# Kernel tuning notes

Hardware: AMD Instinct MI355X
Metric: run time of the kernel (lower is better)

The kernel has to match this reference:

```python
import jax, jax.numpy as jnp
import numpy as np

B, T, C, H = 1, 2048, 1024, 16
K = C // H


def _ln(x, g, b):
    m = x.mean(-1, keepdims=True)
    v = ((x - m) ** 2).mean(-1, keepdims=True)
    return (x - m) * jax.lax.rsqrt(v + 1e-5) * g + b


def setup_inputs() -> dict:
    key = jax.random.key(0)
    ks = jax.random.split(key, 16)
    n = lambda k, s, sc=1.0: jax.random.normal(k, s, jnp.float32) * sc
    u = lambda k, s: jax.random.uniform(k, s, jnp.float32)
    ws = C ** -0.5
    return {
        "x": n(ks[0], (B, T, C)),
        "shift_state": n(ks[1], (B, C)),
        "time_maa_x": u(ks[2], (1, 1, C)),
        "time_maa_r": u(ks[3], (1, 1, C)),
        "time_maa_k": u(ks[4], (1, 1, C)),
        "time_maa_v": u(ks[5], (1, 1, C)),
        "time_maa_w1": n(ks[6], (C, 96), 0.01),
        "time_maa_w2": n(ks[7], (3, 32, C), 0.01),
        "headavg_w1": n(ks[8], (C, 4 * 2 * H), 0.01),
        "headavg_w2": n(ks[9], (4, 2 * H, H), 0.01),
        "w_r": n(ks[10], (C, C), ws),
        "w_k": n(ks[11], (C, C), ws),
        "w_v": n(ks[12], (C, C), ws),
        "w_o": n(ks[13], (C, C), ws),
        "ln_r_g": jnp.ones((C,)), "ln_r_b": jnp.zeros((C,)),
        "ln_k_g": jnp.ones((C,)), "ln_k_b": jnp.zeros((C,)),
        "ln_v_g": jnp.ones((C,)), "ln_v_b": jnp.zeros((C,)),
        "ln_x_g": jnp.ones((C,)), "ln_x_b": jnp.zeros((C,)),
    }


def reference(x, shift_state, time_maa_x, time_maa_r, time_maa_k, time_maa_v,
              time_maa_w1, time_maa_w2, headavg_w1, headavg_w2,
              w_r, w_k, w_v, w_o,
              ln_r_g, ln_r_b, ln_k_g, ln_k_b, ln_v_g, ln_v_b, ln_x_g, ln_x_b):
    Bs, Ts, Cs = x.shape
    Hh = headavg_w2.shape[-1]
    Kk = Cs // Hh

    # token shift
    dxprev = jnp.concatenate([shift_state[:, None, :], x[:, :-1]], axis=1) - x

    # LoRA token-shift mixing
    xxx = jnp.tanh((x + dxprev * time_maa_x) @ time_maa_w1)       # [B,T,3*32]
    mix = jnp.einsum('btnd,ndc->nbtc', xxx.reshape(Bs, Ts, 3, -1), time_maa_w2)
    mq, mk, mv = mix[0], mix[1], mix[2]
    xq = x + dxprev * (time_maa_r + mq)
    xk = x + dxprev * (time_maa_k + mk)
    xv = x + dxprev * (time_maa_v + mv)

    q = _ln(xq @ w_r, ln_r_g, ln_r_b).reshape(Bs, Ts, Hh, Kk).transpose(0, 2, 1, 3)
    k = _ln(xk @ w_k, ln_k_g, ln_k_b).reshape(Bs, Ts, Hh, Kk).transpose(0, 2, 1, 3)
    v = _ln(xv @ w_v, ln_v_g, ln_v_b).reshape(Bs, Ts, Hh, Kk).transpose(0, 2, 1, 3)

    # per-head LoRA score mixing coefficients
    ha = jnp.tanh(x @ headavg_w1).reshape(Bs, Ts, 4, -1)          # [B,T,4,2H]
    hm = jnp.einsum('btnd,ndh->nbth', ha, headavg_w2) / Hh        # [4,B,T,H]
    pre_q, pre_k, post_q, post_k = hm[0], hm[1], hm[2], hm[3]

    scale = Kk ** -0.5
    y = jnp.einsum('bhtk,bhsk->bhts', q * scale, k)               # [B,H,T,S]
    y = y + jnp.einsum('bhts,bth->bts', y, pre_q)[:, None]
    y = y + jnp.einsum('bhts,bsh->bts', y, pre_k)[:, None]

    # causal ALiBi bias
    rel = (jnp.arange(Ts)[:, None] - jnp.arange(Ts)[None, :]).astype(x.dtype)
    slopes = (2.0 ** (-8.0 * jnp.arange(1, Hh + 1, dtype=x.dtype) / Hh))
    bias = jnp.where(rel >= 0, -slopes[:, None, None] * rel, jnp.asarray(-1e9, x.dtype))
    y = y + bias[None]

    y = jax.nn.softmax(y, axis=-1)
    y = y + jnp.einsum('bhts,bth->bts', y, post_q)[:, None]
    y = y + jnp.einsum('bhts,bsh->bts', y, post_k)[:, None]

    out = jnp.einsum('bhts,bhsv->bhtv', y, v).transpose(0, 2, 1, 3).reshape(Bs, Ts, Cs)
    out = _ln(out, ln_x_g, ln_x_b) @ w_o
    return out
```

## Files before the change

kernel.cpp:

```cpp
#include <hip/hip_runtime.h>
#include <cstdint>
#include <cstddef>


#define C_DIM 1024
#define HEADS 16
#define TTL 32
#define STL 32
#define SCHUNK 256
#define PADS 40
#define EPS_STR 36

typedef unsigned short ushort_t;
typedef __attribute__((ext_vector_type(8))) short bf16x8;
typedef __attribute__((ext_vector_type(4))) float f32x4;

#define MFMA16(a, b, c) __builtin_amdgcn_mfma_f32_16x16x32_bf16(a, b, c, 0, 0, 0)

__device__ __forceinline__ unsigned int f2bf_u(float f) {
  unsigned int u = __float_as_uint(f);
  return (u + 0x7fffu + ((u >> 16) & 1u)) >> 16;
}
__device__ __forceinline__ float bf2f(ushort_t u) {
  return __uint_as_float(((unsigned int)u) << 16);
}
__device__ __forceinline__ void pack4(ushort_t* dst, float x0, float x1,
                                      float x2, float x3) {
  uint2 v;
  v.x = f2bf_u(x0) | (f2bf_u(x1) << 16);
  v.y = f2bf_u(x2) | (f2bf_u(x3) << 16);
  *(uint2*)dst = v;
}
__device__ __forceinline__ void mlmerge(float& M, float& L, float m2, float l2) {
  float nm = fmaxf(M, m2);
  float ea = (M  <= -1e29f) ? 0.f : __expf(M - nm);
  float eb = (m2 <= -1e29f) ? 0.f : __expf(m2 - nm);
  L = L * ea + l2 * eb;
  M = nm;
}

__global__ __launch_bounds__(256) void prep_kernel(
    const float* __restrict__ x, const float* __restrict__ shift,
    const float* __restrict__ maa_x,
    float* __restrict__ dxprev, ushort_t* __restrict__ zbf,
    ushort_t* __restrict__ xbf)
{
  const int t = blockIdx.x;
  const int c = threadIdx.x * 4;
  const size_t base = (size_t)t * C_DIM + c;
  const float4 xc = *(const float4*)&x[base];
  const float4 xp = (t == 0) ? *(const float4*)&shift[c]
                             : *(const float4*)&x[base - C_DIM];
  const float4 mx = *(const float4*)&maa_x[c];
  float4 d;
  d.x = xp.x - xc.x; d.y = xp.y - xc.y; d.z = xp.z - xc.z; d.w = xp.w - xc.w;
  *(float4*)&dxprev[base] = d;
  pack4(&zbf[base], xc.x + d.x*mx.x, xc.y + d.y*mx.y,
        xc.z + d.z*mx.z, xc.w + d.w*mx.w);
  pack4(&xbf[base], xc.x, xc.y, xc.z, xc.w);
}

__global__ __launch_bounds__(256) void wlora_prep(
    const float* __restrict__ w1, const float* __restrict__ hw1,
    ushort_t* __restrict__ wlt)
{
  __shared__ float tile[32][33];
  const int k0 = blockIdx.x*32, j0 = blockIdx.y*32;
  const int r = threadIdx.x >> 3, c4 = (threadIdx.x & 7) * 4;
  const float* W = (j0 < 96) ? w1 : hw1;
  const int stride = (j0 < 96) ? 96 : 128;
  const int jo = (j0 < 96) ? j0 : j0 - 96;
  const float4 v = *(const float4*)&W[(size_t)(k0+r)*stride + jo + c4];
  tile[r][c4+0] = v.x; tile[r][c4+1] = v.y;
  tile[r][c4+2] = v.z; tile[r][c4+3] = v.w;
  __syncthreads();
  pack4(&wlt[(size_t)(j0+r)*C_DIM + k0 + c4],
        tile[c4+0][r], tile[c4+1][r], tile[c4+2][r], tile[c4+3][r]);
}

__global__ __launch_bounds__(64) void lora_gemm(
    const ushort_t* __restrict__ zbf, const ushort_t* __restrict__ xbf,
    const ushort_t* __restrict__ wlt, float* __restrict__ xxx,
    float* __restrict__ ha)
{
  const int nt = blockIdx.y;
  const int bm = blockIdx.x * 32;
  const ushort_t* A = (nt < 3) ? zbf : xbf;
  const int wrow = nt * 32;
  const int lane = threadIdx.x;
  const int l15 = lane & 15, g = lane >> 4;
  f32x4 acc[2][2];
  #pragma unroll
  for (int i = 0; i < 2; i++)
    #pragma unroll
    for (int j = 0; j < 2; j++) acc[i][j] = (f32x4){0.f,0.f,0.f,0.f};
  bf16x8 a0[2], b0[2], a1[2], b1[2];
  #define LLA(dst, kk) { \
    dst[0] = *(const bf16x8*)&A[(size_t)(bm + l15)*C_DIM + (kk) + g*8]; \
    dst[1] = *(const bf16x8*)&A[(size_t)(bm + 16 + l15)*C_DIM + (kk) + g*8]; }
  #define LLB(dst, kk) { \
    dst[0] = *(const bf16x8*)&wlt[(size_t)(wrow + l15)*C_DIM + (kk) + g*8]; \
    dst[1] = *(const bf16x8*)&wlt[(size_t)(wrow + 16 + l15)*C_DIM + (kk) + g*8]; }
  LLA(a0, 0); LLB(b0, 0);
  for (int k0 = 0; k0 < C_DIM; k0 += 64) {
    LLA(a1, k0+32); LLB(b1, k0+32);
    #pragma unroll
    for (int i = 0; i < 2; i++)
      #pragma unroll
      for (int j = 0; j < 2; j++) acc[i][j] = MFMA16(a0[i], b0[j], acc[i][j]);
    if (k0 + 64 < C_DIM) { LLA(a0, k0+64); LLB(b0, k0+64); }
    #pragma unroll
    for (int i = 0; i < 2; i++)
      #pragma unroll
      for (int j = 0; j < 2; j++) acc[i][j] = MFMA16(a1[i], b1[j], acc[i][j]);
  }
  #undef LLA
  #undef LLB
  #pragma unroll
  for (int i = 0; i < 2; i++)
    #pragma unroll
    for (int j = 0; j < 2; j++)
      #pragma unroll
      for (int r = 0; r < 4; r++) {
        const int t = bm + i*16 + g*4 + r;
        const int col = wrow + j*16 + l15;
        const float val = tanhf(acc[i][j][r]);
        if (nt < 3) xxx[(size_t)t*96 + col] = val;
        else        ha[(size_t)t*128 + col - 96] = val;
      }
}

__global__ __launch_bounds__(256) void mix_kernel(
    const float* __restrict__ x, const float* __restrict__ dxp,
    const float* __restrict__ xxx,
    const float* __restrict__ maa_r, const float* __restrict__ maa_k,
    const float* __restrict__ maa_v, const float* __restrict__ w2,
    ushort_t* __restrict__ xq, ushort_t* __restrict__ xk,
    ushort_t* __restrict__ xv)
{
  __shared__ float xs[8][96];
  const int t0 = blockIdx.x * 8;
  const int tid = threadIdx.x;
  #pragma unroll
  for (int i = 0; i < 3; i++) {
    const int u = tid + i*256;
    if (u < 768) {
      const int r = u / 96, cc = u % 96;
      xs[r][cc] = xxx[(size_t)(t0+r)*96 + cc];
    }
  }
  __syncthreads();
  const int c = tid * 4;
  float4 xc[8], dx[8];
  #pragma unroll
  for (int r = 0; r < 8; r++) {
    xc[r] = *(const float4*)&x[(size_t)(t0+r)*C_DIM + c];
    dx[r] = *(const float4*)&dxp[(size_t)(t0+r)*C_DIM + c];
  }
  const float* maas[3] = {maa_r, maa_k, maa_v};
  ushort_t* outs[3] = {xq, xk, xv};
  #pragma unroll
  for (int n = 0; n < 3; n++) {
    const float4 mv = *(const float4*)&maas[n][c];
    float m[8][4];
    #pragma unroll
    for (int r = 0; r < 8; r++) {
      m[r][0] = mv.x; m[r][1] = mv.y; m[r][2] = mv.z; m[r][3] = mv.w;
    }
    #pragma unroll 8
    for (int d = 0; d < 32; d++) {
      const float4 w = *(const float4*)&w2[((size_t)n*32 + d)*C_DIM + c];
      #pragma unroll
      for (int r = 0; r < 8; r++) {
        const float xv2 = xs[r][n*32 + d];
        m[r][0] += xv2*w.x; m[r][1] += xv2*w.y;
        m[r][2] += xv2*w.z; m[r][3] += xv2*w.w;
      }
    }
    #pragma unroll
    for (int r = 0; r < 8; r++)
      pack4(&outs[n][(size_t)(t0+r)*C_DIM + c],
            xc[r].x + dx[r].x*m[r][0], xc[r].y + dx[r].y*m[r][1],
            xc[r].z + dx[r].z*m[r][2], xc[r].w + dx[r].w*m[r][3]);
  }
}

__global__ __launch_bounds__(256) void hm_kernel(
    const float* __restrict__ ha, const float* __restrict__ hw2,
    float* __restrict__ hm, int T)
{
  const int t = blockIdx.x*4 + (threadIdx.x >> 6);
  const int u = threadIdx.x & 63;
  const int n = u >> 4, h = u & 15;
  float s = 0.f;
  #pragma unroll 8
  for (int d = 0; d < 32; d++)
    s += ha[(size_t)t*128 + n*32 + d] * hw2[(size_t)(n*32 + d)*16 + h];
  hm[((size_t)n*T + t)*16 + h] = s * (1.f/16.f);
}

__global__ __launch_bounds__(256) void wprep_kernel(
    const float* __restrict__ w0, const float* __restrict__ w1,
    const float* __restrict__ w2, const float* __restrict__ w3,
    ushort_t* __restrict__ o0, ushort_t* __restrict__ o1,
    ushort_t* __restrict__ o2, ushort_t* __restrict__ o3)
{
  const float* W; ushort_t* O;
  if (blockIdx.z == 0)      { W = w0; O = o0; }
  else if (blockIdx.z == 1) { W = w1; O = o1; }
  else if (blockIdx.z == 2) { W = w2; O = o2; }
  else                      { W = w3; O = o3; }
  __shared__ float tile[32][33];
  const int k0 = blockIdx.x*32, n0 = blockIdx.y*32;
  const int r = threadIdx.x >> 3, c4 = (threadIdx.x & 7) * 4;
  const float4 v = *(const float4*)&W[(size_t)(k0+r)*C_DIM + n0 + c4];
  tile[r][c4+0] = v.x; tile[r][c4+1] = v.y;
  tile[r][c4+2] = v.z; tile[r][c4+3] = v.w;
  __syncthreads();
  pack4(&O[(size_t)(n0+r)*C_DIM + k0 + c4],
        tile[c4+0][r], tile[c4+1][r], tile[c4+2][r], tile[c4+3][r]);
}

__global__ __launch_bounds__(64) void gemm_bf16(
    const ushort_t* __restrict__ A, const ushort_t* __restrict__ Bt,
    float* __restrict__ Cm)
{
  const int bid = blockIdx.x;
  const int bn = (bid & 15) * 64;
  const int bm = (bid >> 4) * 32;
  const int lane = threadIdx.x;
  const int l15 = lane & 15, g = lane >> 4;
  f32x4 acc[2][4];
  #pragma unroll
  for (int i = 0; i < 2; i++)
    #pragma unroll
    for (int j = 0; j < 4; j++) acc[i][j] = (f32x4){0.f,0.f,0.f,0.f};
  bf16x8 a0[2], b0[4], a1[2], b1[4];
  #define LGA(dst, kk) { \
    _Pragma("unroll") \
    for (int i = 0; i < 2; i++) \
      dst[i] = *(const bf16x8*)&A[(size_t)(bm + i*16 + l15)*C_DIM + (kk) + g*8]; }
  #define LGB(dst, kk) { \
    _Pragma("unroll") \
    for (int j = 0; j < 4; j++) \
      dst[j] = *(const bf16x8*)&Bt[(size_t)(bn + j*16 + l15)*C_DIM + (kk) + g*8]; }
  LGA(a0, 0); LGB(b0, 0);
  for (int k0 = 0; k0 < C_DIM; k0 += 64) {
    LGA(a1, k0+32); LGB(b1, k0+32);
    #pragma unroll
    for (int i = 0; i < 2; i++)
      #pragma unroll
      for (int j = 0; j < 4; j++) acc[i][j] = MFMA16(a0[i], b0[j], acc[i][j]);
    if (k0 + 64 < C_DIM) { LGA(a0, k0+64); LGB(b0, k0+64); }
    #pragma unroll
    for (int i = 0; i < 2; i++)
      #pragma unroll
      for (int j = 0; j < 4; j++) acc[i][j] = MFMA16(a1[i], b1[j], acc[i][j]);
  }
  #undef LGA
  #undef LGB
  #pragma unroll
  for (int i = 0; i < 2; i++)
    #pragma unroll
    for (int j = 0; j < 4; j++)
      #pragma unroll
      for (int r = 0; r < 4; r++)
        Cm[(size_t)(bm + i*16 + g*4 + r)*C_DIM + bn + j*16 + l15] = acc[i][j][r];
}

__global__ __launch_bounds__(256) void ln_rows(
    const float* __restrict__ in, ushort_t* __restrict__ outp,
    const float* __restrict__ g, const float* __restrict__ b, float scale)
{
  __shared__ float red[4];
  const int t = blockIdx.x;
  const int tid = threadIdx.x;
  const int c = tid*4;
  const float4 v = *(const float4*)&in[(size_t)t*C_DIM + c];
  float s = v.x+v.y+v.z+v.w;
  #pragma unroll
  for (int off = 32; off > 0; off >>= 1) s += __shfl_down(s, off, 64);
  if ((tid & 63) == 0) red[tid >> 6] = s;
  __syncthreads();
  const float mean = (red[0]+red[1]+red[2]+red[3]) * (1.0f/C_DIM);
  __syncthreads();
  const float d0 = v.x-mean, d1 = v.y-mean, d2 = v.z-mean, d3 = v.w-mean;
  float q = d0*d0 + d1*d1 + d2*d2 + d3*d3;
  #pragma unroll
  for (int off = 32; off > 0; off >>= 1) q += __shfl_down(q, off, 64);
  if ((tid & 63) == 0) red[tid >> 6] = q;
  __syncthreads();
  const float var = (red[0]+red[1]+red[2]+red[3]) * (1.0f/C_DIM);
  const float rstd = rsqrtf(var + 1e-5f);
  const float4 gv = *(const float4*)&g[c];
  const float4 bv = *(const float4*)&b[c];
  pack4(outp + (size_t)t*C_DIM + c,
        (d0*rstd*gv.x + bv.x)*scale, (d1*rstd*gv.y + bv.y)*scale,
        (d2*rstd*gv.z + bv.z)*scale, (d3*rstd*gv.w + bv.w)*scale);
}

__global__ __launch_bounds__(256) void vtrans_kernel(
    const ushort_t* __restrict__ vbf, ushort_t* __restrict__ Vt, int T)
{
  __shared__ ushort_t tile[32][36];
  const int t0 = blockIdx.x*32, c0 = blockIdx.y*32;
  const int r = threadIdx.x >> 3, c4 = (threadIdx.x & 7) * 4;
  const uint2 raw = *(const uint2*)&vbf[(size_t)(t0+r)*C_DIM + c0 + c4];
  tile[r][c4+0] = (ushort_t)(raw.x & 0xffffu);
  tile[r][c4+1] = (ushort_t)(raw.x >> 16);
  tile[r][c4+2] = (ushort_t)(raw.y & 0xffffu);
  tile[r][c4+3] = (ushort_t)(raw.y >> 16);
  __syncthreads();
  uint2 w;
  w.x = (unsigned)tile[c4+0][r] | ((unsigned)tile[c4+1][r] << 16);
  w.y = (unsigned)tile[c4+2][r] | ((unsigned)tile[c4+3][r] << 16);
  *(uint2*)&Vt[(size_t)(c0+r)*T + t0 + c4] = w;
}

__global__ __launch_bounds__(1024) void attn_stats(
    const ushort_t* __restrict__ qbf, const ushort_t* __restrict__ kbf,
    const float* __restrict__ hmb, float* __restrict__ part_m,
    float* __restrict__ part_l, int T)
{
  __shared__ ushort_t ybuf[HEADS*TTL*PADS];
  __shared__ float ep[TTL*EPS_STR];

  const int bid = blockIdx.x;
  const int sc = bid & 7;
  const int tb = (T/TTL) - 1 - (bid >> 3);
  const int t0 = tb * TTL;
  const int sbeg = sc * SCHUNK;
  if (sbeg >= t0 + TTL) return;
  const int send = (sbeg + SCHUNK < t0 + TTL) ? (sbeg + SCHUNK) : (t0 + TTL);

  const int tid = threadIdx.x;
  const int h = tid >> 6;
  const int lane = tid & 63;
  const int l15 = lane & 15, g = lane >> 4;
  const int tc = tid >> 5, scell = tid & 31;

  bf16x8 qf[2][2];
  #pragma unroll
  for (int th = 0; th < 2; th++)
    #pragma unroll
    for (int kc = 0; kc < 2; kc++)
      qf[th][kc] = *(const bf16x8*)
          &qbf[(size_t)(t0 + th*16 + l15)*C_DIM + h*64 + kc*32 + g*8];
  const float slope = exp2f(-0.5f * (float)(h + 1));
  float mrun[2] = {-1e30f, -1e30f}, lrun[2] = {0.f, 0.f};

  for (int s1 = sbeg; s1 < send; s1 += STL) {
    f32x4 acc[2][2];
    #pragma unroll
    for (int sh = 0; sh < 2; sh++)
      #pragma unroll
      for (int th = 0; th < 2; th++) acc[sh][th] = (f32x4){0.f,0.f,0.f,0.f};
    #pragma unroll
    for (int sh = 0; sh < 2; sh++)
      #pragma unroll
      for (int kc = 0; kc < 2; kc++) {
        const bf16x8 kf = *(const bf16x8*)
            &kbf[(size_t)(s1 + sh*16 + l15)*C_DIM + h*64 + kc*32 + g*8];
        #pragma unroll
        for (int th = 0; th < 2; th++)
          acc[sh][th] = MFMA16(kf, qf[th][kc], acc[sh][th]);
      }
    #pragma unroll
    for (int sh = 0; sh < 2; sh++)
      #pragma unroll
      for (int th = 0; th < 2; th++)
        pack4(&ybuf[(h*TTL + th*16 + l15)*PADS + sh*16 + g*4],
              acc[sh][th][0], acc[sh][th][1], acc[sh][th][2], acc[sh][th][3]);
    __syncthreads();
    {
      float hq[16], hk[16];
      #pragma unroll
      for (int q4 = 0; q4 < 4; q4++) {
        *(float4*)&hq[q4*4] = *(const float4*)&hmb[((size_t)0*T + t0+tc)*16 + q4*4];
        *(float4*)&hk[q4*4] = *(const float4*)&hmb[((size_t)1*T + s1+scell)*16 + q4*4];
      }
      float a = 0.f, b0 = 0.f, spk = 0.f;
      #pragma unroll
      for (int h2 = 0; h2 < 16; h2++) {
        const float y = bf2f(ybuf[(h2*TTL + tc)*PADS + scell]);
        a += y * hq[h2];
        b0 += y * hk[h2];
        spk += hk[h2];
      }
      ep[tc*EPS_STR + scell] = a*(1.f + spk) + b0;
    }
    __syncthreads();
    #pragma unroll
    for (int th = 0; th < 2; th++) {
      const int t = t0 + th*16 + l15;
      #pragma unroll
      for (int sh = 0; sh < 2; sh++)
        #pragma unroll
        for (int r = 0; r < 4; r++) {
          const int s = s1 + sh*16 + g*4 + r;
          if (s <= t) {
            const float y3 = acc[sh][th][r]
                + ep[(th*16 + l15)*EPS_STR + sh*16 + g*4 + r]
                - slope * (float)(t - s);
            const float d = y3 - mrun[th];
            if (d > 0.f) { lrun[th] = lrun[th]*__expf(-d) + 1.f; mrun[th] = y3; }
            else lrun[th] += __expf(d);
          }
        }
    }
    __syncthreads();
  }
  #pragma unroll
  for (int th = 0; th < 2; th++) {
    float M = mrun[th], L = lrun[th];
    #pragma unroll
    for (int mask = 16; mask < 64; mask <<= 1) {
      const float M2 = __shfl_xor(M, mask, 64);
      const float L2 = __shfl_xor(L, mask, 64);
      mlmerge(M, L, M2, L2);
    }
    if (g == 0) {
      part_m[(size_t)(sc*HEADS + h)*T + t0 + th*16 + l15] = M;
      part_l[(size_t)(sc*HEADS + h)*T + t0 + th*16 + l15] = L;
    }
  }
}

__global__ __launch_bounds__(256) void ml_combine(
    const float* __restrict__ part_m, const float* __restrict__ part_l,
    float* __restrict__ m_fin, float* __restrict__ linv, int T)
{
  const int idx = blockIdx.x*256 + threadIdx.x;
  const int t = idx & (T - 1);
  const int t0 = t & ~(TTL - 1);
  const int nsc = (t0 + TTL + SCHUNK - 1) / SCHUNK;
  float M = -1e30f, L = 0.f;
  for (int sc = 0; sc < nsc; sc++)
    mlmerge(M, L, part_m[(size_t)sc*HEADS*T + idx],
            part_l[(size_t)sc*HEADS*T + idx]);
  m_fin[idx] = M;
  linv[idx] = 1.f / L;
}

__global__ __launch_bounds__(1024) void attn_apply(
    const ushort_t* __restrict__ qbf, const ushort_t* __restrict__ kbf,
    const ushort_t* __restrict__ Vt, const float* __restrict__ hmb,
    const float* __restrict__ m_fin, const float* __restrict__ linv,
    float* __restrict__ P, int T)
{
  __shared__ ushort_t ybuf[HEADS*TTL*PADS];
  __shared__ float ep[TTL*EPS_STR];

  const int bid = blockIdx.x;
  const int sc = bid & 7;
  const int tb = (T/TTL) - 1 - (bid >> 3);
  const int t0 = tb * TTL;
  const int sbeg = sc * SCHUNK;
  if (sbeg >= t0 + TTL) return;
  const int send = (sbeg + SCHUNK < t0 + TTL) ? (sbeg + SCHUNK) : (t0 + TTL);
  const int prow0 = T*sc - 128*sc*(sc-1) - SCHUNK*sc;

  const int tid = threadIdx.x;
  const int h = tid >> 6;
  const int lane = tid & 63;
  const int l15 = lane & 15, g = lane >> 4;
  const int tc = tid >> 5, scell = tid & 31;

  bf16x8 qf[2][2];
  float mt[2], li[2];
  #pragma unroll
  for (int th = 0; th < 2; th++) {
    #pragma unroll
    for (int kc = 0; kc < 2; kc++)
      qf[th][kc] = *(const bf16x8*)
          &qbf[(size_t)(t0 + th*16 + l15)*C_DIM + h*64 + kc*32 + g*8];
    mt[th] = m_fin[(size_t)h*T + t0 + th*16 + l15];
    li[th] = linv[(size_t)h*T + t0 + th*16 + l15];
  }
  const float slope = exp2f(-0.5f * (float)(h + 1));
  f32x4 oacc[2][4];
  #pragma unroll
  for (int th = 0; th < 2; th++)
    #pragma unroll
    for (int vf = 0; vf < 4; vf++) oacc[th][vf] = (f32x4){0.f,0.f,0.f,0.f};

  for (int s1 = sbeg; s1 < send; s1 += STL) {
    f32x4 acc[2][2];
    #pragma unroll
    for (int sh = 0; sh < 2; sh++)
      #pragma unroll
      for (int th = 0; th < 2; th++) acc[sh][th] = (f32x4){0.f,0.f,0.f,0.f};
    #pragma unroll
    for (int sh = 0; sh < 2; sh++)
      #pragma unroll
      for (int kc = 0; kc < 2; kc++) {
        const bf16x8 kf = *(const bf16x8*)
            &kbf[(size_t)(s1 + sh*16 + l15)*C_DIM + h*64 + kc*32 + g*8];
        #pragma unroll
        for (int th = 0; th < 2; th++)
          acc[sh][th] = MFMA16(kf, qf[th][kc], acc[sh][th]);
      }
    #pragma unroll
    for (int sh = 0; sh < 2; sh++)
      #pragma unroll
      for (int th = 0; th < 2; th++)
        pack4(&ybuf[(h*TTL + th*16 + l15)*PADS + sh*16 + g*4],
              acc[sh][th][0], acc[sh][th][1], acc[sh][th][2], acc[sh][th][3]);
    __syncthreads();
    {
      float hq[16], hk[16];
      #pragma unroll
      for (int q4 = 0; q4 < 4; q4++) {
        *(float4*)&hq[q4*4] = *(const float4*)&hmb[((size_t)0*T + t0+tc)*16 + q4*4];
        *(float4*)&hk[q4*4] = *(const float4*)&hmb[((size_t)1*T + s1+scell)*16 + q4*4];
      }
      float a = 0.f, b0 = 0.f, spk = 0.f;
      #pragma unroll
      for (int h2 = 0; h2 < 16; h2++) {
        const float y = bf2f(ybuf[(h2*TTL + tc)*PADS + scell]);
        a += y * hq[h2];
        b0 += y * hk[h2];
        spk += hk[h2];
      }
      ep[tc*EPS_STR + scell] = a*(1.f + spk) + b0;
    }
    __syncthreads();
    #pragma unroll
    for (int th = 0; th < 2; th++) {
      const int t = t0 + th*16 + l15;
      #pragma unroll
      for (int sh = 0; sh < 2; sh++)
        #pragma unroll
        for (int r = 0; r < 4; r++) {
          const int s = s1 + sh*16 + g*4 + r;
          float p = 0.f;
          if (s <= t) {
            const float y3 = acc[sh][th][r]
                + ep[(th*16 + l15)*EPS_STR + sh*16 + g*4 + r]
                - slope * (float)(t - s);
            p = __expf(y3 - mt[th]) * li[th];
          }
          acc[sh][th][r] = p;
        }
    }
    #pragma unroll
    for (int sh = 0; sh < 2; sh++)
      #pragma unroll
      for (int th = 0; th < 2; th++)
        pack4(&ybuf[(h*TTL + th*16 + l15)*PADS + sh*16 + g*4],
              acc[sh][th][0], acc[sh][th][1], acc[sh][th][2], acc[sh][th][3]);
    __syncthreads();
    {
      float hq[16], hk[16];
      #pragma unroll
      for (int q4 = 0; q4 < 4; q4++) {
        *(float4*)&hq[q4*4] = *(const float4*)&hmb[((size_t)2*T + t0+tc)*16 + q4*4];
        *(float4*)&hk[q4*4] = *(const float4*)&hmb[((size_t)3*T + s1+scell)*16 + q4*4];
      }
      float cmx = 0.f, d0 = 0.f, spo = 0.f;
      #pragma unroll
      for (int h2 = 0; h2 < 16; h2++) {
        const float p = bf2f(ybuf[(h2*TTL + tc)*PADS + scell]);
        cmx += p * hq[h2];
        d0 += p * hk[h2];
        spo += hk[h2];
      }
      ep[tc*EPS_STR + scell] = cmx*(1.f + spo) + d0;
    }
    __syncthreads();
    #pragma unroll
    for (int sh = 0; sh < 2; sh++)
      #pragma unroll
      for (int th = 0; th < 2; th++) {
        const int ebase = (th*16 + l15)*EPS_STR + sh*16 + g*4;
        pack4(&ybuf[(h*TTL + th*16 + l15)*PADS + sh*16 + g*4],
              acc[sh][th][0] + ep[ebase+0], acc[sh][th][1] + ep[ebase+1],
              acc[sh][th][2] + ep[ebase+2], acc[sh][th][3] + ep[ebase+3]);
      }
    __syncthreads();
    #pragma unroll
    for (int th = 0; th < 2; th++) {
      const bf16x8 pa = *(const bf16x8*)&ybuf[(h*TTL + th*16 + l15)*PADS + g*8];
      #pragma unroll
      for (int vf = 0; vf < 4; vf++) {
        const bf16x8 vv = *(const bf16x8*)
            &Vt[(size_t)(h*64 + vf*16 + l15)*T + s1 + g*8];
        oacc[th][vf] = MFMA16(pa, vv, oacc[th][vf]);
      }
    }
    __syncthreads();
  }
  #pragma unroll
  for (int th = 0; th < 2; th++)
    #pragma unroll
    for (int vf = 0; vf < 4; vf++)
      #pragma unroll
      for (int r = 0; r < 4; r++)
        P[(size_t)(prow0 + t0 + th*16 + g*4 + r)*C_DIM
          + h*64 + vf*16 + l15] = oacc[th][vf][r];
}

__global__ __launch_bounds__(256) void reduce_ln(
    const float* __restrict__ P, ushort_t* __restrict__ outp,
    const float* __restrict__ g, const float* __restrict__ b, int T)
{
  __shared__ float red[4];
  const int t = blockIdx.x;
  const int tid = threadIdx.x;
  const int c = tid*4;
  const int nsc = (t >> 8) + 1;
  float4 v = make_float4(0.f, 0.f, 0.f, 0.f);
  int off = 0;
  for (int sc = 0; sc < nsc; sc++) {
    const int row = off + t - sc*SCHUNK;
    const float4 pv = *(const float4*)&P[(size_t)row*C_DIM + c];
    v.x += pv.x; v.y += pv.y; v.z += pv.z; v.w += pv.w;
    off += T - SCHUNK*sc;
  }
  float s = v.x+v.y+v.z+v.w;
  #pragma unroll
  for (int o = 32; o > 0; o >>= 1) s += __shfl_down(s, o, 64);
  if ((tid & 63) == 0) red[tid >> 6] = s;
  __syncthreads();
  const float mean = (red[0]+red[1]+red[2]+red[3]) * (1.0f/C_DIM);
  __syncthreads();
  const float d0 = v.x-mean, d1 = v.y-mean, d2 = v.z-mean, d3 = v.w-mean;
  float q = d0*d0 + d1*d1 + d2*d2 + d3*d3;
  #pragma unroll
  for (int o = 32; o > 0; o >>= 1) q += __shfl_down(q, o, 64);
  if ((tid & 63) == 0) red[tid >> 6] = q;
  __syncthreads();
  const float var = (red[0]+red[1]+red[2]+red[3]) * (1.0f/C_DIM);
  const float rstd = rsqrtf(var + 1e-5f);
  const float4 gv = *(const float4*)&g[c];
  const float4 bv = *(const float4*)&b[c];
  pack4(outp + (size_t)t*C_DIM + c,
        d0*rstd*gv.x + bv.x, d1*rstd*gv.y + bv.y,
        d2*rstd*gv.z + bv.z, d3*rstd*gv.w + bv.w);
}

extern "C" void kernel_launch(void* const* d_in, const int* in_sizes, int n_in,
                              void* d_out, int out_size, void* d_ws, size_t ws_size,
                              hipStream_t stream)
{
  const float* x      = (const float*)d_in[0];
  const float* shift  = (const float*)d_in[1];
  const float* maa_x  = (const float*)d_in[2];
  const float* maa_r  = (const float*)d_in[3];
  const float* maa_k  = (const float*)d_in[4];
  const float* maa_v  = (const float*)d_in[5];
  const float* w1     = (const float*)d_in[6];
  const float* w2     = (const float*)d_in[7];
  const float* hw1    = (const float*)d_in[8];
  const float* hw2    = (const float*)d_in[9];
  const float* w_r    = (const float*)d_in[10];
  const float* w_k    = (const float*)d_in[11];
  const float* w_v    = (const float*)d_in[12];
  const float* w_o    = (const float*)d_in[13];
  const float* ln_r_g = (const float*)d_in[14];
  const float* ln_r_b = (const float*)d_in[15];
  const float* ln_k_g = (const float*)d_in[16];
  const float* ln_k_b = (const float*)d_in[17];
  const float* ln_v_g = (const float*)d_in[18];
  const float* ln_v_b = (const float*)d_in[19];
  const float* ln_x_g = (const float*)d_in[20];
  const float* ln_x_b = (const float*)d_in[21];

  const int T = in_sizes[0] / C_DIM;
  const size_t MM = (size_t)T * C_DIM;
  const size_t HF = MM / 2;

  float* ws = (float*)d_ws;
  float*    P      = ws;
  float*    dxprev = ws;
  ushort_t* zbf    = (ushort_t*)(ws + MM);
  ushort_t* xbf    = (ushort_t*)(ws + MM + HF);
  float*    gtmp   = ws + 2*MM;
  ushort_t* xqb    = (ushort_t*)(ws + 3*MM);
  ushort_t* xkb    = (ushort_t*)(ws + 3*MM + HF);
  ushort_t* xvb    = (ushort_t*)(ws + 4*MM);
  float* base2 = ws + 4*MM + HF;
  ushort_t* qbf = (ushort_t*)(base2 + 0*HF);
  ushort_t* kbf = (ushort_t*)(base2 + 1*HF);
  ushort_t* vbf = (ushort_t*)(base2 + 2*HF);
  ushort_t* Vt  = (ushort_t*)(base2 + 3*HF);
  ushort_t* wtr = (ushort_t*)(base2 + 4*HF);
  ushort_t* wtk = wtr + (size_t)C_DIM*C_DIM;
  ushort_t* wtv = wtk + (size_t)C_DIM*C_DIM;
  ushort_t* wto = wtv + (size_t)C_DIM*C_DIM;
  float* after_w = base2 + 4*HF + (size_t)2*C_DIM*C_DIM;
  ushort_t* wlt = (ushort_t*)after_w;
  float* xxx    = after_w + 131072;
  float* ha     = xxx + (size_t)T*96;
  float* hmb    = ha + (size_t)T*128;
  float* part_m = hmb + (size_t)4*T*16;
  float* part_l = part_m + (size_t)8*HEADS*T;
  float* m_fin  = part_l + (size_t)8*HEADS*T;
  float* linv   = m_fin + (size_t)HEADS*T;
  ushort_t* abf = (ushort_t*)(linv + (size_t)HEADS*T);

  prep_kernel<<<T, 256, 0, stream>>>(x, shift, maa_x, dxprev, zbf, xbf);
  wlora_prep<<<dim3(C_DIM/32, 7), 256, 0, stream>>>(w1, hw1, wlt);
  lora_gemm<<<dim3(T/32, 7), 64, 0, stream>>>(zbf, xbf, wlt, xxx, ha);
  mix_kernel<<<T/8, 256, 0, stream>>>(x, dxprev, xxx, maa_r, maa_k, maa_v, w2,
                                      xqb, xkb, xvb);
  hm_kernel<<<T/4, 256, 0, stream>>>(ha, hw2, hmb, T);
  wprep_kernel<<<dim3(32, 32, 4), 256, 0, stream>>>(
      w_r, w_k, w_v, w_o, wtr, wtk, wtv, wto);

  const int ggemm = (T/32) * (C_DIM/64);
  gemm_bf16<<<ggemm, 64, 0, stream>>>(xqb, wtr, gtmp);
  ln_rows<<<T, 256, 0, stream>>>(gtmp, qbf, ln_r_g, ln_r_b, 0.125f);
  gemm_bf16<<<ggemm, 64, 0, stream>>>(xkb, wtk, gtmp);
  ln_rows<<<T, 256, 0, stream>>>(gtmp, kbf, ln_k_g, ln_k_b, 1.0f);
  gemm_bf16<<<ggemm, 64, 0, stream>>>(xvb, wtv, gtmp);
  ln_rows<<<T, 256, 0, stream>>>(gtmp, vbf, ln_v_g, ln_v_b, 1.0f);
  vtrans_kernel<<<dim3(T/32, C_DIM/32), 256, 0, stream>>>(vbf, Vt, T);

  attn_stats<<<(T/TTL)*8, 1024, 0, stream>>>(qbf, kbf, hmb, part_m, part_l, T);
  ml_combine<<<(HEADS*T)/256, 256, 0, stream>>>(part_m, part_l, m_fin, linv, T);
  attn_apply<<<(T/TTL)*8, 1024, 0, stream>>>(
      qbf, kbf, Vt, hmb, m_fin, linv, P, T);

  reduce_ln<<<T, 256, 0, stream>>>(P, abf, ln_x_g, ln_x_b, T);
  gemm_bf16<<<ggemm, 64, 0, stream>>>(abf, wto, (float*)d_out);
}
```

Before: 572.1 us.

## Restructure attention kernels to 16-query tiles with two heads per wave

The attention stats and apply kernels now use 16-query tiles and 512-thread blocks, with each wave handling two heads. The per-chunk head-mixing coefficients and their row sums are staged once in shared memory instead of being reloaded from global memory every step. The apply kernel also issues its V-fragment loads early and drops the trailing barrier to cut synchronisation. The aim is higher occupancy and less redundant global traffic, at the cost of more shared memory and twice as many blocks.

```diff
diff --git a/kernel.cpp b/kernel.cpp
--- a/kernel.cpp
+++ b/kernel.cpp
@@ -5,11 +5,10 @@
 
 #define C_DIM 1024
 #define HEADS 16
-#define TTL 32
-#define STL 32
-#define SCHUNK 256
+#define TQ 16
+#define SCH 256
 #define PADS 40
-#define EPS_STR 36
+#define EPS 33
 
 typedef unsigned short ushort_t;
 typedef __attribute__((ext_vector_type(8))) short bf16x8;
@@ -317,102 +316,111 @@
   *(uint2*)&Vt[(size_t)(c0+r)*T + t0 + c4] = w;
 }
 
-__global__ __launch_bounds__(1024) void attn_stats(
+__global__ __launch_bounds__(512, 4) void attn_stats(
     const ushort_t* __restrict__ qbf, const ushort_t* __restrict__ kbf,
     const float* __restrict__ hmb, float* __restrict__ part_m,
     float* __restrict__ part_l, int T)
 {
-  __shared__ ushort_t ybuf[HEADS*TTL*PADS];
-  __shared__ float ep[TTL*EPS_STR];
-
-  const int bid = blockIdx.x;
-  const int sc = bid & 7;
-  const int tb = (T/TTL) - 1 - (bid >> 3);
-  const int t0 = tb * TTL;
-  const int sbeg = sc * SCHUNK;
-  if (sbeg >= t0 + TTL) return;
-  const int send = (sbeg + SCHUNK < t0 + TTL) ? (sbeg + SCHUNK) : (t0 + TTL);
+  __shared__ ushort_t ybuf[HEADS*TQ*PADS];
+  __shared__ float ep[TQ*EPS];
+  __shared__ float hpqf[TQ*16];
+  __shared__ float hpkf[SCH*16];
+  __shared__ float spk_l[SCH];
+
+  const int sc = blockIdx.x;
+  const int tb = (int)gridDim.y - 1 - (int)blockIdx.y;
+  const int t0 = tb * TQ;
+  const int sbeg = sc * SCH;
+  if (sbeg >= t0 + TQ) return;
+  const int send = (sbeg + SCH < t0 + TQ) ? (sbeg + SCH) : (t0 + TQ);
 
   const int tid = threadIdx.x;
-  const int h = tid >> 6;
-  const int lane = tid & 63;
-  const int l15 = lane & 15, g = lane >> 4;
+  const int w = tid >> 6, lane = tid & 63, l15 = lane & 15, g = lane >> 4;
   const int tc = tid >> 5, scell = tid & 31;
 
+  for (int i = tid; i < SCH*16; i += 512)
+    hpkf[i] = hmb[((size_t)1*T + sbeg)*16 + i];
+  if (tid < TQ*16)
+    hpqf[tid] = hmb[((size_t)0*T + t0)*16 + tid];
+  if (tid < SCH) {
+    const float* src = hmb + ((size_t)1*T + sbeg + tid)*16;
+    float s = 0.f;
+    #pragma unroll
+    for (int q4 = 0; q4 < 4; q4++) {
+      const float4 v = *(const float4*)&src[q4*4];
+      s += v.x + v.y + v.z + v.w;
+    }
+    spk_l[tid] = s;
+  }
+
+  const int hh[2] = {w, w + 8};
   bf16x8 qf[2][2];
-  #pragma unroll
-  for (int th = 0; th < 2; th++)
+  float slope[2];
+  #pragma unroll
+  for (int hd = 0; hd < 2; hd++) {
     #pragma unroll
     for (int kc = 0; kc < 2; kc++)
-      qf[th][kc] = *(const bf16x8*)
-          &qbf[(size_t)(t0 + th*16 + l15)*C_DIM + h*64 + kc*32 + g*8];
-  const float slope = exp2f(-0.5f * (float)(h + 1));
+      qf[hd][kc] = *(const bf16x8*)
+          &qbf[(size_t)(t0 + l15)*C_DIM + hh[hd]*64 + kc*32 + g*8];
+    slope[hd] = exp2f(-0.5f * (float)(hh[hd] + 1));
+  }
   float mrun[2] = {-1e30f, -1e30f}, lrun[2] = {0.f, 0.f};
 
-  for (int s1 = sbeg; s1 < send; s1 += STL) {
+  for (int s1 = sbeg; s1 < send; s1 += 32) {
     f32x4 acc[2][2];
     #pragma unroll
-    for (int sh = 0; sh < 2; sh++)
-      #pragma unroll
-      for (int th = 0; th < 2; th++) acc[sh][th] = (f32x4){0.f,0.f,0.f,0.f};
-    #pragma unroll
-    for (int sh = 0; sh < 2; sh++)
-      #pragma unroll
-      for (int kc = 0; kc < 2; kc++) {
-        const bf16x8 kf = *(const bf16x8*)
-            &kbf[(size_t)(s1 + sh*16 + l15)*C_DIM + h*64 + kc*32 + g*8];
+    for (int hd = 0; hd < 2; hd++)
+      #pragma unroll
+      for (int sh = 0; sh < 2; sh++) acc[hd][sh] = (f32x4){0.f,0.f,0.f,0.f};
+    #pragma unroll
+    for (int hd = 0; hd < 2; hd++) {
+      #pragma unroll
+      for (int sh = 0; sh < 2; sh++)
         #pragma unroll
-        for (int th = 0; th < 2; th++)
-          acc[sh][th] = MFMA16(kf, qf[th][kc], acc[sh][th]);
-      }
-    #pragma unroll
-    for (int sh = 0; sh < 2; sh++)
-      #pragma unroll
-      for (int th = 0; th < 2; th++)
-        pack4(&ybuf[(h*TTL + th*16 + l15)*PADS + sh*16 + g*4],
-              acc[sh][th][0], acc[sh][th][1], acc[sh][th][2], acc[sh][th][3]);
+        for (int kc = 0; kc < 2; kc++) {
+          const bf16x8 kf = *(const bf16x8*)
+              &kbf[(size_t)(s1 + sh*16 + l15)*C_DIM + hh[hd]*64 + kc*32 + g*8];
+          acc[hd][sh] = MFMA16(kf, qf[hd][kc], acc[hd][sh]);
+        }
+      #pragma unroll
+      for (int sh = 0; sh < 2; sh++)
+        pack4(&ybuf[(size_t)(hh[hd]*TQ + l15)*PADS + sh*16 + g*4],
+              acc[hd][sh][0], acc[hd][sh][1], acc[hd][sh][2], acc[hd][sh][3]);
+    }
     __syncthreads();
     {
-      float hq[16], hk[16];
-      #pragma unroll
-      for (int q4 = 0; q4 < 4; q4++) {
-        *(float4*)&hq[q4*4] = *(const float4*)&hmb[((size_t)0*T + t0+tc)*16 + q4*4];
-        *(float4*)&hk[q4*4] = *(const float4*)&hmb[((size_t)1*T + s1+scell)*16 + q4*4];
+      const int so = s1 - sbeg + scell;
+      float a = 0.f, b0 = 0.f;
+      #pragma unroll
+      for (int h2 = 0; h2 < 16; h2++) {
+        const float y = bf2f(ybuf[(h2*TQ + tc)*PADS + scell]);
+        a  += y * hpqf[tc*16 + h2];
+        b0 += y * hpkf[so*16 + h2];
       }
-      float a = 0.f, b0 = 0.f, spk = 0.f;
-      #pragma unroll
-      for (int h2 = 0; h2 < 16; h2++) {
-        const float y = bf2f(ybuf[(h2*TTL + tc)*PADS + scell]);
-        a += y * hq[h2];
-        b0 += y * hk[h2];
-        spk += hk[h2];
-      }
-      ep[tc*EPS_STR + scell] = a*(1.f + spk) + b0;
+      ep[tc*EPS + scell] = a*(1.f + spk_l[so]) + b0;
     }
     __syncthreads();
     #pragma unroll
-    for (int th = 0; th < 2; th++) {
-      const int t = t0 + th*16 + l15;
+    for (int hd = 0; hd < 2; hd++) {
+      const int t = t0 + l15;
       #pragma unroll
       for (int sh = 0; sh < 2; sh++)
         #pragma unroll
         for (int r = 0; r < 4; r++) {
           const int s = s1 + sh*16 + g*4 + r;
           if (s <= t) {
-            const float y3 = acc[sh][th][r]
-                + ep[(th*16 + l15)*EPS_STR + sh*16 + g*4 + r]
-                - slope * (float)(t - s);
-            const float d = y3 - mrun[th];
-            if (d > 0.f) { lrun[th] = lrun[th]*__expf(-d) + 1.f; mrun[th] = y3; }
-            else lrun[th] += __expf(d);
+            const float y3 = acc[hd][sh][r] + ep[l15*EPS + sh*16 + g*4 + r]
+                - slope[hd]*(float)(t - s);
+            const float d = y3 - mrun[hd];
+            if (d > 0.f) { lrun[hd] = lrun[hd]*__expf(-d) + 1.f; mrun[hd] = y3; }
+            else lrun[hd] += __expf(d);
           }
         }
     }
-    __syncthreads();
-  }
-  #pragma unroll
-  for (int th = 0; th < 2; th++) {
-    float M = mrun[th], L = lrun[th];
+  }
+  #pragma unroll
+  for (int hd = 0; hd < 2; hd++) {
+    float M = mrun[hd], L = lrun[hd];
     #pragma unroll
     for (int mask = 16; mask < 64; mask <<= 1) {
       const float M2 = __shfl_xor(M, mask, 64);
@@ -420,8 +428,8 @@
       mlmerge(M, L, M2, L2);
     }
     if (g == 0) {
-      part_m[(size_t)(sc*HEADS + h)*T + t0 + th*16 + l15] = M;
-      part_l[(size_t)(sc*HEADS + h)*T + t0 + th*16 + l15] = L;
+      part_m[(size_t)(sc*HEADS + hh[hd])*T + t0 + l15] = M;
+      part_l[(size_t)(sc*HEADS + hh[hd])*T + t0 + l15] = L;
     }
   }
 }
@@ -432,8 +440,7 @@
 {
   const int idx = blockIdx.x*256 + threadIdx.x;
   const int t = idx & (T - 1);
-  const int t0 = t & ~(TTL - 1);
-  const int nsc = (t0 + TTL + SCHUNK - 1) / SCHUNK;
+  const int nsc = (t >> 8) + 1;
   float M = -1e30f, L = 0.f;
   for (int sc = 0; sc < nsc; sc++)
     mlmerge(M, L, part_m[(size_t)sc*HEADS*T + idx],
@@ -442,162 +449,167 @@
   linv[idx] = 1.f / L;
 }
 
-__global__ __launch_bounds__(1024) void attn_apply(
+__global__ __launch_bounds__(512, 4) void attn_apply(
     const ushort_t* __restrict__ qbf, const ushort_t* __restrict__ kbf,
     const ushort_t* __restrict__ Vt, const float* __restrict__ hmb,
     const float* __restrict__ m_fin, const float* __restrict__ linv,
     float* __restrict__ P, int T)
 {
-  __shared__ ushort_t ybuf[HEADS*TTL*PADS];
-  __shared__ float ep[TTL*EPS_STR];
-
-  const int bid = blockIdx.x;
-  const int sc = bid & 7;
-  const int tb = (T/TTL) - 1 - (bid >> 3);
-  const int t0 = tb * TTL;
-  const int sbeg = sc * SCHUNK;
-  if (sbeg >= t0 + TTL) return;
-  const int send = (sbeg + SCHUNK < t0 + TTL) ? (sbeg + SCHUNK) : (t0 + TTL);
-  const int prow0 = T*sc - 128*sc*(sc-1) - SCHUNK*sc;
+  __shared__ ushort_t ybuf[HEADS*TQ*PADS];
+  __shared__ float ep[TQ*EPS];
+  __shared__ float hpqf[TQ*16], hoqf[TQ*16];
+  __shared__ float hpkf[SCH*16], hokf[SCH*16];
+  __shared__ float spk_l[SCH], spo_l[SCH];
+
+  const int sc = blockIdx.x;
+  const int tb = (int)gridDim.y - 1 - (int)blockIdx.y;
+  const int t0 = tb * TQ;
+  const int sbeg = sc * SCH;
+  if (sbeg >= t0 + TQ) return;
+  const int send = (sbeg + SCH < t0 + TQ) ? (sbeg + SCH) : (t0 + TQ);
+  const int prow0 = T*sc - 128*sc*(sc-1) - SCH*sc;
 
   const int tid = threadIdx.x;
-  const int h = tid >> 6;
-  const int lane = tid & 63;
-  const int l15 = lane & 15, g = lane >> 4;
+  const int w = tid >> 6, lane = tid & 63, l15 = lane & 15, g = lane >> 4;
   const int tc = tid >> 5, scell = tid & 31;
 
+  for (int i = tid; i < SCH*16; i += 512) {
+    hpkf[i] = hmb[((size_t)1*T + sbeg)*16 + i];
+    hokf[i] = hmb[((size_t)3*T + sbeg)*16 + i];
+  }
+  if (tid < TQ*16) {
+    hpqf[tid] = hmb[((size_t)0*T + t0)*16 + tid];
+    hoqf[tid] = hmb[((size_t)2*T + t0)*16 + tid];
+  }
+  {
+    const int s_l = tid & 255;
+    const float* src = hmb + ((size_t)((tid < 256) ? 1 : 3)*T + sbeg + s_l)*16;
+    float s = 0.f;
+    #pragma unroll
+    for (int q4 = 0; q4 < 4; q4++) {
+      const float4 v = *(const float4*)&src[q4*4];
+      s += v.x + v.y + v.z + v.w;
+    }
+    if (tid < 256) spk_l[s_l] = s; else spo_l[s_l] = s;
+  }
+
+  const int hh[2] = {w, w + 8};
   bf16x8 qf[2][2];
-  float mt[2], li[2];
-  #pragma unroll
-  for (int th = 0; th < 2; th++) {
+  float mt[2], li[2], slope[2];
+  #pragma unroll
+  for (int hd = 0; hd < 2; hd++) {
     #pragma unroll
     for (int kc = 0; kc < 2; kc++)
-      qf[th][kc] = *(const bf16x8*)
-          &qbf[(size_t)(t0 + th*16 + l15)*C_DIM + h*64 + kc*32 + g*8];
-    mt[th] = m_fin[(size_t)h*T + t0 + th*16 + l15];
-    li[th] = linv[(size_t)h*T + t0 + th*16 + l15];
-  }
-  const float slope = exp2f(-0.5f * (float)(h + 1));
+      qf[hd][kc] = *(const bf16x8*)
+          &qbf[(size_t)(t0 + l15)*C_DIM + hh[hd]*64 + kc*32 + g*8];
+    mt[hd] = m_fin[(size_t)hh[hd]*T + t0 + l15];
+    li[hd] = linv[(size_t)hh[hd]*T + t0 + l15];
+    slope[hd] = exp2f(-0.5f * (float)(hh[hd] + 1));
+  }
   f32x4 oacc[2][4];
   #pragma unroll
-  for (int th = 0; th < 2; th++)
-    #pragma unroll
-    for (int vf = 0; vf < 4; vf++) oacc[th][vf] = (f32x4){0.f,0.f,0.f,0.f};
-
-  for (int s1 = sbeg; s1 < send; s1 += STL) {
+  for (int hd = 0; hd < 2; hd++)
+    #pragma unroll
+    for (int vf = 0; vf < 4; vf++) oacc[hd][vf] = (f32x4){0.f,0.f,0.f,0.f};
+
+  for (int s1 = sbeg; s1 < send; s1 += 32) {
     f32x4 acc[2][2];
     #pragma unroll
-    for (int sh = 0; sh < 2; sh++)
-      #pragma unroll
-      for (int th = 0; th < 2; th++) acc[sh][th] = (f32x4){0.f,0.f,0.f,0.f};
-    #pragma unroll
-    for (int sh = 0; sh < 2; sh++)
-      #pragma unroll
-      for (int kc = 0; kc < 2; kc++) {
-        const bf16x8 kf = *(const bf16x8*)
-            &kbf[(size_t)(s1 + sh*16 + l15)*C_DIM + h*64 + kc*32 + g*8];
+    for (int hd = 0; hd < 2; hd++)
+      #pragma unroll
+      for (int sh = 0; sh < 2; sh++) acc[hd][sh] = (f32x4){0.f,0.f,0.f,0.f};
+    #pragma unroll
+    for (int hd = 0; hd < 2; hd++) {
+      #pragma unroll
+      for (int sh = 0; sh < 2; sh++)
         #pragma unroll
-        for (int th = 0; th < 2; th++)
-          acc[sh][th] = MFMA16(kf, qf[th][kc], acc[sh][th]);
-      }
-    #pragma unroll
-    for (int sh = 0; sh < 2; sh++)
-      #pragma unroll
-      for (int th = 0; th < 2; th++)
-        pack4(&ybuf[(h*TTL + th*16 + l15)*PADS + sh*16 + g*4],
-              acc[sh][th][0], acc[sh][th][1], acc[sh][th][2], acc[sh][th][3]);
+        for (int kc = 0; kc < 2; kc++) {
+          const bf16x8 kf = *(const bf16x8*)
+              &kbf[(size_t)(s1 + sh*16 + l15)*C_DIM + hh[hd]*64 + kc*32 + g*8];
+          acc[hd][sh] = MFMA16(kf, qf[hd][kc], acc[hd][sh]);
+        }
+      #pragma unroll
+      for (int sh = 0; sh < 2; sh++)
+        pack4(&ybuf[(size_t)(hh[hd]*TQ + l15)*PADS + sh*16 + g*4],
+              acc[hd][sh][0], acc[hd][sh][1], acc[hd][sh][2], acc[hd][sh][3]);
+    }
     __syncthreads();
     {
-      float hq[16], hk[16];
-      #pragma unroll
-      for (int q4 = 0; q4 < 4; q4++) {
-        *(float4*)&hq[q4*4] = *(const float4*)&hmb[((size_t)0*T + t0+tc)*16 + q4*4];
-        *(float4*)&hk[q4*4] = *(const float4*)&hmb[((size_t)1*T + s1+scell)*16 + q4*4];
+      const int so = s1 - sbeg + scell;
+      float a = 0.f, b0 = 0.f;
+      #pragma unroll
+      for (int h2 = 0; h2 < 16; h2++) {
+        const float y = bf2f(ybuf[(h2*TQ + tc)*PADS + scell]);
+        a  += y * hpqf[tc*16 + h2];
+        b0 += y * hpkf[so*16 + h2];
       }
-      float a = 0.f, b0 = 0.f, spk = 0.f;
-      #pragma unroll
-      for (int h2 = 0; h2 < 16; h2++) {
-        const float y = bf2f(ybuf[(h2*TTL + tc)*PADS + scell]);
-        a += y * hq[h2];
-        b0 += y * hk[h2];
-        spk += hk[h2];
-      }
-      ep[tc*EPS_STR + scell] = a*(1.f + spk) + b0;
+      ep[tc*EPS + scell] = a*(1.f + spk_l[so]) + b0;
     }
     __syncthreads();
     #pragma unroll
-    for (int th = 0; th < 2; th++) {
-      const int t = t0 + th*16 + l15;
-      #pragma unroll
-      for (int sh = 0; sh < 2; sh++)
+    for (int hd = 0; hd < 2; hd++) {
+      const int t = t0 + l15;
+      #pragma unroll
+      for (int sh = 0; sh < 2; sh++) {
         #pragma unroll
         for (int r = 0; r < 4; r++) {
           const int s = s1 + sh*16 + g*4 + r;
           float p = 0.f;
           if (s <= t) {
-            const float y3 = acc[sh][th][r]
-                + ep[(th*16 + l15)*EPS_STR + sh*16 + g*4 + r]
-                - slope * (float)(t - s);
-            p = __expf(y3 - mt[th]) * li[th];
+            const float y3 = acc[hd][sh][r] + ep[l15*EPS + sh*16 + g*4 + r]
+                - slope[hd]*(float)(t - s);
+            p = __expf(y3 - mt[hd]) * li[hd];
           }
-          acc[sh][th][r] = p;
+          acc[hd][sh][r] = p;
         }
-    }
-    #pragma unroll
-    for (int sh = 0; sh < 2; sh++)
-      #pragma unroll
-      for (int th = 0; th < 2; th++)
-        pack4(&ybuf[(h*TTL + th*16 + l15)*PADS + sh*16 + g*4],
-              acc[sh][th][0], acc[sh][th][1], acc[sh][th][2], acc[sh][th][3]);
+        pack4(&ybuf[(size_t)(hh[hd]*TQ + l15)*PADS + sh*16 + g*4],
+              acc[hd][sh][0], acc[hd][sh][1], acc[hd][sh][2], acc[hd][sh][3]);
+      }
+    }
+    bf16x8 vv[2][4];
+    #pragma unroll
+    for (int hd = 0; hd < 2; hd++)
+      #pragma unroll
+      for (int vf = 0; vf < 4; vf++)
+        vv[hd][vf] = *(const bf16x8*)
+            &Vt[(size_t)(hh[hd]*64 + vf*16 + l15)*T + s1 + g*8];
     __syncthreads();
     {
-      float hq[16], hk[16];
-      #pragma unroll
-      for (int q4 = 0; q4 < 4; q4++) {
-        *(float4*)&hq[q4*4] = *(const float4*)&hmb[((size_t)2*T + t0+tc)*16 + q4*4];
-        *(float4*)&hk[q4*4] = *(const float4*)&hmb[((size_t)3*T + s1+scell)*16 + q4*4];
+      const int so = s1 - sbeg + scell;
+      float cm = 0.f, d0 = 0.f;
+      #pragma unroll
+      for (int h2 = 0; h2 < 16; h2++) {
+        const float pv = bf2f(ybuf[(h2*TQ + tc)*PADS + scell]);
+        cm += pv * hoqf[tc*16 + h2];
+        d0 += pv * hokf[so*16 + h2];
       }
-      float cmx = 0.f, d0 = 0.f, spo = 0.f;
-      #pragma unroll
-      for (int h2 = 0; h2 < 16; h2++) {
-        const float p = bf2f(ybuf[(h2*TTL + tc)*PADS + scell]);
-        cmx += p * hq[h2];
-        d0 += p * hk[h2];
-        spo += hk[h2];
+      ep[tc*EPS + scell] = cm*(1.f + spo_l[so]) + d0;
+    }
+    __syncthreads();
+    #pragma unroll
+    for (int hd = 0; hd < 2; hd++) {
+      #pragma unroll
+      for (int sh = 0; sh < 2; sh++) {
+        const int eb = l15*EPS + sh*16 + g*4;
+        pack4(&ybuf[(size_t)(hh[hd]*TQ + l15)*PADS + sh*16 + g*4],
+              acc[hd][sh][0] + ep[eb+0], acc[hd][sh][1] + ep[eb+1],
+              acc[hd][sh][2] + ep[eb+2], acc[hd][sh][3] + ep[eb+3]);
       }
-      ep[tc*EPS_STR + scell] = cmx*(1.f + spo) + d0;
-    }
-    __syncthreads();
-    #pragma unroll
-    for (int sh = 0; sh < 2; sh++)
-      #pragma unroll
-      for (int th = 0; th < 2; th++) {
-        const int ebase = (th*16 + l15)*EPS_STR + sh*16 + g*4;
-        pack4(&ybuf[(h*TTL + th*16 + l15)*PADS + sh*16 + g*4],
-              acc[sh][th][0] + ep[ebase+0], acc[sh][th][1] + ep[ebase+1],
-              acc[sh][th][2] + ep[ebase+2], acc[sh][th][3] + ep[ebase+3]);
-      }
-    __syncthreads();
-    #pragma unroll
-    for (int th = 0; th < 2; th++) {
-      const bf16x8 pa = *(const bf16x8*)&ybuf[(h*TTL + th*16 + l15)*PADS + g*8];
-      #pragma unroll
-      for (int vf = 0; vf < 4; vf++) {
-        const bf16x8 vv = *(const bf16x8*)
-            &Vt[(size_t)(h*64 + vf*16 + l15)*T + s1 + g*8];
-        oacc[th][vf] = MFMA16(pa, vv, oacc[th][vf]);
-      }
-    }
-    __syncthreads();
-  }
-  #pragma unroll
-  for (int th = 0; th < 2; th++)
+      const bf16x8 pa = *(const bf16x8*)
+          &ybuf[(size_t)(hh[hd]*TQ + l15)*PADS + g*8];
+      #pragma unroll
+      for (int vf = 0; vf < 4; vf++)
+        oacc[hd][vf] = MFMA16(pa, vv[hd][vf], oacc[hd][vf]);
+    }
+  }
+  #pragma unroll
+  for (int hd = 0; hd < 2; hd++)
     #pragma unroll
     for (int vf = 0; vf < 4; vf++)
       #pragma unroll
       for (int r = 0; r < 4; r++)
-        P[(size_t)(prow0 + t0 + th*16 + g*4 + r)*C_DIM
-          + h*64 + vf*16 + l15] = oacc[th][vf][r];
+        P[(size_t)(prow0 + t0 + g*4 + r)*C_DIM + hh[hd]*64 + vf*16 + l15]
+            = oacc[hd][vf][r];
 }
 
 __global__ __launch_bounds__(256) void reduce_ln(
@@ -612,10 +624,10 @@
   float4 v = make_float4(0.f, 0.f, 0.f, 0.f);
   int off = 0;
   for (int sc = 0; sc < nsc; sc++) {
-    const int row = off + t - sc*SCHUNK;
+    const int row = off + t - sc*SCH;
     const float4 pv = *(const float4*)&P[(size_t)row*C_DIM + c];
     v.x += pv.x; v.y += pv.y; v.z += pv.z; v.w += pv.w;
-    off += T - SCHUNK*sc;
+    off += T - SCH*sc;
   }
   float s = v.x+v.y+v.z+v.w;
   #pragma unroll
@@ -717,9 +729,10 @@
   ln_rows<<<T, 256, 0, stream>>>(gtmp, vbf, ln_v_g, ln_v_b, 1.0f);
   vtrans_kernel<<<dim3(T/32, C_DIM/32), 256, 0, stream>>>(vbf, Vt, T);
 
-  attn_stats<<<(T/TTL)*8, 1024, 0, stream>>>(qbf, kbf, hmb, part_m, part_l, T);
+  attn_stats<<<dim3(8, T/TQ), 512, 0, stream>>>(
+      qbf, kbf, hmb, part_m, part_l, T);
   ml_combine<<<(HEADS*T)/256, 256, 0, stream>>>(part_m, part_l, m_fin, linv, T);
-  attn_apply<<<(T/TTL)*8, 1024, 0, stream>>>(
+  attn_apply<<<dim3(8, T/TQ), 512, 0, stream>>>(
       qbf, kbf, Vt, hmb, m_fin, linv, P, T);
 
   reduce_ln<<<T, 256, 0, stream>>>(P, abf, ln_x_g, ln_x_b, T);
```

Result: faster. 525.7 us (-8.1%).
